# Performance work log

Hardware: AMD Instinct MI355X
Metric: run time of the kernel (lower is better)

The kernel has to match this reference:

```python
import jax, jax.numpy as jnp
import numpy as np

N_CODES, CODE_DIM = 1024, 256

def setup_inputs() -> dict:
    key = jax.random.key(0)
    k1, k2 = jax.random.split(key)
    z = jax.random.normal(k1, (32, 256, 32, 32), dtype=jnp.float32)
    # nn.init.uniform_(codebook.weight, -1/n_codes, 1/n_codes)
    codebook = jax.random.uniform(k2, (N_CODES, CODE_DIM), dtype=jnp.float32,
                                  minval=-1.0 / N_CODES, maxval=1.0 / N_CODES)
    return {"z": z, "codebook": codebook}

def reference(z, codebook):
    b, c, h, w = z.shape
    beta = 0.25
    z_flat = jnp.transpose(z, (0, 2, 3, 1)).reshape(-1, c)  # [B*H*W, C]
    z_sq = jnp.sum(z_flat * z_flat, axis=1, keepdims=True)   # [N,1]
    e_sq = jnp.sum(codebook * codebook, axis=1)              # [K]
    ze = z_flat @ codebook.T                                 # [N,K]
    dists = z_sq + e_sq[None, :] - 2.0 * ze
    indices = jnp.argmin(dists, axis=1)                      # [N]
    z_q = codebook[indices].reshape(b, h, w, c)
    z_q = jnp.transpose(z_q, (0, 3, 1, 2))                   # [B,C,H,W]
    z_q_st = z + jax.lax.stop_gradient(z_q - z)
    commitment = jnp.mean((jax.lax.stop_gradient(z) - z_q) ** 2)
    codebook_loss = jnp.mean((z - jax.lax.stop_gradient(z_q)) ** 2)
    vq_loss = codebook_loss + beta * commitment
    return z_q_st, vq_loss, indices.reshape(b, h, w)
```

## Files before the change

### kernel.cpp

```cpp
#include <hip/hip_runtime.h>
#include <math.h>

#define NROWS   32768
#define CDIM    256
#define KCODES  1024
#define ZQ_ELEMS 8388608

typedef short  bshort8 __attribute__((ext_vector_type(8)));
typedef float  f32x4   __attribute__((ext_vector_type(4)));

#define ESQ_OFF   0
#define ZSQH_OFF  1024
#define IDX_OFF   459776
#define LIST_OFF  492544
#define CNT_OFF   525312
#define ACC_OFF   525313
#define BHI_OFF   525328
#define BLO_OFF   656400


#define MARGIN_ABS 1.0e-4f

__device__ __forceinline__ ushort f2bf(float f) {
    union { float f; uint u; } v; v.f = f;
    uint lsb = (v.u >> 16) & 1u;
    return (ushort)((v.u + 0x7fffu + lsb) >> 16);
}
__device__ __forceinline__ float bf2f(ushort b) {
    union { uint u; float f; } v; v.u = ((uint)b) << 16;
    return v.f;
}

__global__ __launch_bounds__(256) void prep_kernel(const float* __restrict__ cb,
                                                   uint* __restrict__ Bhi, uint* __restrict__ Blo,
                                                   float* __restrict__ esq,
                                                   float* __restrict__ cbT) {
    const int blk = blockIdx.x, tid = threadIdx.x;
    if (blk < 128) {
        int F = blk * 256 + tid;
        int ct = F >> 9, ks = (F >> 6) & 7, ln = F & 63;
        int code = ct * 16 + (ln & 15);
        int k0 = ks * 32 + ((ln >> 4) << 3);
        const float* p = cb + (size_t)code * CDIM + k0;
        float4 va = *(const float4*)p;
        float4 vb = *(const float4*)(p + 4);
        float v[8] = {va.x, va.y, va.z, va.w, vb.x, vb.y, vb.z, vb.w};
        uint h[4], l[4];
#pragma unroll
        for (int d = 0; d < 4; ++d) {
            ushort h0 = f2bf(v[2*d]);   float r0 = v[2*d]   - bf2f(h0);
            ushort h1 = f2bf(v[2*d+1]); float r1 = v[2*d+1] - bf2f(h1);
            h[d] = (uint)h0 | ((uint)h1 << 16);
            l[d] = (uint)f2bf(r0) | ((uint)f2bf(r1) << 16);
        }
        *(uint4*)(Bhi + (size_t)F * 4) = make_uint4(h[0], h[1], h[2], h[3]);
        *(uint4*)(Blo + (size_t)F * 4) = make_uint4(l[0], l[1], l[2], l[3]);
    } else if (blk < 132) {
        int k = (blk - 128) * 256 + tid;
        const float* p = cb + (size_t)k * CDIM;
        float half_[2];
        for (int h = 0; h < 2; ++h) {
            const float* q = p + h * 128;
            float r8[8];
#pragma unroll
            for (int j = 0; j < 8; ++j) { float v = q[j]; r8[j] = __fmul_rn(v, v); }
            for (int i = 8; i < 128; i += 8) {
#pragma unroll
                for (int j = 0; j < 8; ++j) {
                    float v = q[i + j];
                    r8[j] = __fadd_rn(r8[j], __fmul_rn(v, v));
                }
            }
            half_[h] = __fadd_rn(__fadd_rn(__fadd_rn(r8[0], r8[1]), __fadd_rn(r8[2], r8[3])),
                                 __fadd_rn(__fadd_rn(r8[4], r8[5]), __fadd_rn(r8[6], r8[7])));
        }
        esq[k] = __fadd_rn(half_[0], half_[1]);
    } else {
        int base = (blk - 132) * 4096 + tid;
#pragma unroll
        for (int i = 0; i < 16; ++i) {
            int idx = base + i * 256;
            cbT[idx] = cb[(size_t)(idx & 1023) * CDIM + (idx >> 10)];
        }
    }
}

__global__ __launch_bounds__(512, 2) void main_mfma(const float* __restrict__ z,
                                                    const uint* __restrict__ Bhi,
                                                    const uint* __restrict__ Blo,
                                                    const float* __restrict__ esq,
                                                    float* __restrict__ zsqh,
                                                    float* __restrict__ oidxf,
                                                    int* __restrict__ idx_i,
                                                    int* __restrict__ list,
                                                    int* __restrict__ count) {
    __shared__ uint a_hi[8][4][64][4];
    __shared__ uint a_lo[8][4][64][4];
    __shared__ uint b_lds[8][2][4][64][4];
    __shared__ float esq_s[1024];
    __shared__ float zsq_s[64];
    __shared__ float m_b[8][64];
    __shared__ float m_s[8][64];
    __shared__ int   m_i[8][64];

    const int tid  = threadIdx.x;
    const int rg   = blockIdx.x;
    const int b    = rg >> 4;
    const int hw0  = (rg & 15) << 6;
    const int w    = tid >> 6;
    const int lane = tid & 63;

    {
        float2 e2 = *(const float2*)(esq + tid * 2);
        esq_s[tid * 2] = e2.x; esq_s[tid * 2 + 1] = e2.y;
    }

    {
        float* zt = (float*)&b_lds[0][0][0][0][0];
        float r8[8];
        const int zhalf = tid >> 6;
        const int zrow  = tid & 63;
        const int prt   = tid >> 6;
        const int plane = tid & 63;
        const int prow  = (plane & 15) + prt * 16;
        const int pkb   = (plane >> 4) << 3;

        for (int kc = 0; kc < 8; ++kc) {
            __syncthreads();
            {
                int cl = tid >> 4, h4 = tid & 15;
                float4 v = *(const float4*)(z + ((size_t)(b * 256 + kc * 32 + cl) << 10) + hw0 + h4 * 4);
                *(float4*)&zt[cl * 68 + h4 * 4] = v;
            }
            __syncthreads();
            if (tid < 128 && (kc >> 2) == zhalf) {
#pragma unroll
                for (int g = 0; g < 4; ++g)
#pragma unroll
                    for (int j = 0; j < 8; ++j) {
                        float v = zt[(g * 8 + j) * 68 + zrow];
                        float sq = __fmul_rn(v, v);
                        r8[j] = ((kc & 3) == 0 && g == 0) ? sq : __fadd_rn(r8[j], sq);
                    }
            }
            if (tid < 256) {
                uint hh[4], ll[4];
#pragma unroll
                for (int d = 0; d < 4; ++d) {
                    float v0 = zt[(pkb + 2*d)     * 68 + prow];
                    float v1 = zt[(pkb + 2*d + 1) * 68 + prow];
                    ushort x0 = f2bf(v0); float q0 = v0 - bf2f(x0);
                    ushort x1 = f2bf(v1); float q1 = v1 - bf2f(x1);
                    hh[d] = (uint)x0 | ((uint)x1 << 16);
                    ll[d] = (uint)f2bf(q0) | ((uint)f2bf(q1) << 16);
                }
                *(uint4*)&a_hi[kc][prt][plane][0] = make_uint4(hh[0], hh[1], hh[2], hh[3]);
                *(uint4*)&a_lo[kc][prt][plane][0] = make_uint4(ll[0], ll[1], ll[2], ll[3]);
            }
        }
        __syncthreads();
        if (tid < 128) {
            float hs = __fadd_rn(__fadd_rn(__fadd_rn(r8[0], r8[1]), __fadd_rn(r8[2], r8[3])),
                                 __fadd_rn(__fadd_rn(r8[4], r8[5]), __fadd_rn(r8[6], r8[7])));
            zt[zhalf * 64 + zrow] = hs;
            zsqh[zhalf * NROWS + rg * 64 + zrow] = hs;
        }
        __syncthreads();
        if (tid < 64) zsq_s[tid] = __fadd_rn(zt[tid], zt[64 + tid]);
        __syncthreads();
    }

#define GLDS(SRC, DST) __builtin_amdgcn_global_load_lds(                          \
        (const __attribute__((address_space(1))) void*)(SRC),                     \
        (__attribute__((address_space(3))) void*)(DST), 16, 0, 0)

    auto stage = [&](int t) {
        const int cg = t >> 3, ks = t & 7, buf = t & 1;
#pragma unroll
        for (int c = 0; c < 2; ++c) {
            int ct = w * 8 + cg * 2 + c;
            size_t F = ((size_t)(ct * 8 + ks) * 64 + lane);
            GLDS(Bhi + F * 4, &b_lds[w][buf][c * 2 + 0][0][0]);
            GLDS(Blo + F * 4, &b_lds[w][buf][c * 2 + 1][0][0]);
        }
    };

    float best[16], sec[16]; int bidx[16];
#pragma unroll
    for (int s = 0; s < 16; ++s) { best[s] = INFINITY; sec[s] = INFINITY; bidx[s] = 0; }

    f32x4 acc[4][2];

    asm volatile("s_waitcnt vmcnt(0)" ::: "memory");
    stage(0);

    for (int t = 0; t < 32; ++t) {
        const int ks = t & 7, cg = t >> 3, buf = t & 1;
        if (ks == 0) {
#pragma unroll
            for (int rt = 0; rt < 4; ++rt)
#pragma unroll
                for (int c = 0; c < 2; ++c) acc[rt][c] = (f32x4){0.f, 0.f, 0.f, 0.f};
        }
        if (t < 31) {
            stage(t + 1);
            asm volatile("s_waitcnt vmcnt(4)" ::: "memory");
        } else {
            asm volatile("s_waitcnt vmcnt(0)" ::: "memory");
        }
        __builtin_amdgcn_sched_barrier(0);

        {
            bshort8 bh[2], bl[2];
#pragma unroll
            for (int c = 0; c < 2; ++c) {
                bh[c] = *(const bshort8*)&b_lds[w][buf][c * 2 + 0][lane][0];
                bl[c] = *(const bshort8*)&b_lds[w][buf][c * 2 + 1][lane][0];
            }
#pragma unroll
            for (int rt = 0; rt < 4; ++rt) {
                bshort8 ah = *(const bshort8*)&a_hi[ks][rt][lane][0];
                bshort8 al = *(const bshort8*)&a_lo[ks][rt][lane][0];
#pragma unroll
                for (int c = 0; c < 2; ++c) {
                    acc[rt][c] = __builtin_amdgcn_mfma_f32_16x16x32_bf16(al, bh[c], acc[rt][c], 0, 0, 0);
                    acc[rt][c] = __builtin_amdgcn_mfma_f32_16x16x32_bf16(ah, bl[c], acc[rt][c], 0, 0, 0);
                    acc[rt][c] = __builtin_amdgcn_mfma_f32_16x16x32_bf16(ah, bh[c], acc[rt][c], 0, 0, 0);
                }
            }
        }

        if (ks == 7) {
            const int g = lane >> 4, cl = lane & 15;
#pragma unroll
            for (int c = 0; c < 2; ++c) {
                int ct = w * 8 + cg * 2 + c;
                int code = ct * 16 + cl;
                float es = esq_s[code];
#pragma unroll
                for (int rt = 0; rt < 4; ++rt)
#pragma unroll
                    for (int reg = 0; reg < 4; ++reg) {
                        int row_l = rt * 16 + g * 4 + reg;
                        float t1 = __fadd_rn(zsq_s[row_l], es);
                        float dd = __fadd_rn(t1, __fmul_rn(-2.0f, acc[rt][c][reg]));
                        int s = rt * 4 + reg;
                        if (dd < best[s]) { sec[s] = best[s]; best[s] = dd; bidx[s] = code; }
                        else if (dd < sec[s]) sec[s] = dd;
                    }
            }
        }
    }
#undef GLDS

#pragma unroll
    for (int mk = 1; mk <= 8; mk <<= 1) {
#pragma unroll
        for (int s = 0; s < 16; ++s) {
            float ob = __shfl_xor(best[s], mk, 64);
            float os = __shfl_xor(sec[s],  mk, 64);
            int   oi = __shfl_xor(bidx[s], mk, 64);
            float mx = fmaxf(best[s], ob);
            sec[s] = fminf(fminf(sec[s], os), mx);
            if (ob < best[s] || (ob == best[s] && oi < bidx[s])) { best[s] = ob; bidx[s] = oi; }
        }
    }
    if ((lane & 15) == 0) {
        const int g = lane >> 4;
#pragma unroll
        for (int s = 0; s < 16; ++s) {
            int rt = s >> 2, reg = s & 3;
            int row_l = rt * 16 + g * 4 + reg;
            m_b[w][row_l] = best[s]; m_s[w][row_l] = sec[s]; m_i[w][row_l] = bidx[s];
        }
    }
    __syncthreads();
    if (tid < 64) {
        float bb = INFINITY, ss = INFINITY; int bi = 0;
#pragma unroll
        for (int q = 0; q < 8; ++q) {
            float v = m_b[q][tid]; int vi = m_i[q][tid];
            if (v < bb || (v == bb && vi < bi)) { ss = bb; bb = v; bi = vi; }
            else ss = fminf(ss, v);
            ss = fminf(ss, m_s[q][tid]);
        }
        int row = rg * 64 + tid;
        if (ss <= bb + MARGIN_ABS) {
            int p = atomicAdd(count, 1);
            list[p] = row;
        } else {
            oidxf[row] = (float)bi;
            idx_i[row] = bi;
        }
    }
}

__global__ __launch_bounds__(256) void rescan_kernel(const float* __restrict__ z,
                                                     const float* __restrict__ cbT,
                                                     const float* __restrict__ esq,
                                                     const float* __restrict__ zsqh,
                                                     const int* __restrict__ list,
                                                     const int* __restrict__ count,
                                                     float* __restrict__ oidxf,
                                                     int* __restrict__ idx_i) {
    __shared__ float ct_lds[8][1024];
    __shared__ float z_lds[16][256];
    __shared__ float esq_lds[1024];
    const int tid = threadIdx.x, lane = tid & 63, w = tid >> 6;
    const int n = count[0];
#pragma unroll
    for (int i = 0; i < 4; ++i) esq_lds[i * 256 + tid] = esq[i * 256 + tid];

    for (int base = blockIdx.x * 16; base < n; base += gridDim.x * 16) {
        __syncthreads();
        for (int i = 0; i < 16; ++i) {
            int gi = base + i;
            int row = list[gi < n ? gi : n - 1];
            z_lds[i][tid] = z[((size_t)(row >> 10) * 256 + tid) * 1024 + (row & 1023)];
        }

        float acc[4][16];
#pragma unroll
        for (int r = 0; r < 4; ++r)
#pragma unroll
            for (int j = 0; j < 16; ++j) acc[r][j] = 0.0f;

        for (int kt = 0; kt < 32; ++kt) {
            __syncthreads();
#pragma unroll
            for (int u = 0; u < 8; ++u) {
                float4 v = *(const float4*)(cbT + (size_t)(kt * 8 + u) * 1024 + tid * 4);
                *(float4*)&ct_lds[u][tid * 4] = v;
            }
            __syncthreads();
#pragma unroll
            for (int k8 = 0; k8 < 8; ++k8) {
                float4 c[4];
#pragma unroll
                for (int j = 0; j < 4; ++j)
                    c[j] = *(const float4*)&ct_lds[k8][lane * 16 + j * 4];
#pragma unroll
                for (int r = 0; r < 4; ++r) {
                    float zv = z_lds[w * 4 + r][kt * 8 + k8];
                    acc[r][0]  = fmaf(zv, c[0].x, acc[r][0]);
                    acc[r][1]  = fmaf(zv, c[0].y, acc[r][1]);
                    acc[r][2]  = fmaf(zv, c[0].z, acc[r][2]);
                    acc[r][3]  = fmaf(zv, c[0].w, acc[r][3]);
                    acc[r][4]  = fmaf(zv, c[1].x, acc[r][4]);
                    acc[r][5]  = fmaf(zv, c[1].y, acc[r][5]);
                    acc[r][6]  = fmaf(zv, c[1].z, acc[r][6]);
                    acc[r][7]  = fmaf(zv, c[1].w, acc[r][7]);
                    acc[r][8]  = fmaf(zv, c[2].x, acc[r][8]);
                    acc[r][9]  = fmaf(zv, c[2].y, acc[r][9]);
                    acc[r][10] = fmaf(zv, c[2].z, acc[r][10]);
                    acc[r][11] = fmaf(zv, c[2].w, acc[r][11]);
                    acc[r][12] = fmaf(zv, c[3].x, acc[r][12]);
                    acc[r][13] = fmaf(zv, c[3].y, acc[r][13]);
                    acc[r][14] = fmaf(zv, c[3].z, acc[r][14]);
                    acc[r][15] = fmaf(zv, c[3].w, acc[r][15]);
                }
            }
        }

#pragma unroll
        for (int r = 0; r < 4; ++r) {
            int slot = w * 4 + r;
            int gi = base + slot;
            int row = list[gi < n ? gi : n - 1];
            float zs = __fadd_rn(zsqh[row], zsqh[NROWS + row]);
            float bv = INFINITY; int bi = 0;
#pragma unroll
            for (int j = 0; j < 16; ++j) {
                int code = lane * 16 + j;
                float dd = __fadd_rn(__fadd_rn(zs, esq_lds[code]), __fmul_rn(-2.0f, acc[r][j]));
                if (dd < bv) { bv = dd; bi = code; }
            }
#pragma unroll
            for (int mk = 1; mk <= 32; mk <<= 1) {
                float ob = __shfl_xor(bv, mk, 64);
                int   oi = __shfl_xor(bi, mk, 64);
                if (ob < bv || (ob == bv && oi < bi)) { bv = ob; bi = oi; }
            }
            if (lane == 0 && gi < n) { oidxf[row] = (float)bi; idx_i[row] = bi; }
        }
    }
}

__global__ __launch_bounds__(256) void gather_kernel(const float* __restrict__ z,
                                                     const float* __restrict__ cb,
                                                     const int* __restrict__ idx_i,
                                                     float* __restrict__ out0,
                                                     float* __restrict__ accum) {
    int tid   = threadIdx.x;
    int blk   = blockIdx.x;
    int b     = blk >> 5;
    int chunk = (blk >> 3) & 3;
    int cgrp  = blk & 7;
    int hw = chunk * 256 + tid;
    int n  = b * 1024 + hw;
    int code = idx_i[n];
    const float* cp = cb + (size_t)code * CDIM + cgrp * 32;
    float lsum = 0.0f;
    size_t base = (size_t)b * 262144 + hw + (size_t)(cgrp * 32) * 1024;
#pragma unroll
    for (int cc = 0; cc < 8; ++cc) {
        float4 q4 = *(const float4*)(cp + cc * 4);
        float qv[4] = {q4.x, q4.y, q4.z, q4.w};
#pragma unroll
        for (int u = 0; u < 4; ++u) {
            size_t off = base + (size_t)(cc * 4 + u) * 1024;
            float zv = z[off];
            out0[off] = qv[u];
            float dfr = zv - qv[u];
            lsum = fmaf(dfr, dfr, lsum);
        }
    }
#pragma unroll
    for (int mm = 32; mm >= 1; mm >>= 1) lsum += __shfl_down(lsum, mm, 64);
    __shared__ float red[4];
    int wv = tid >> 6, ln = tid & 63;
    if (ln == 0) red[wv] = lsum;
    __syncthreads();
    if (tid == 0) atomicAdd(accum, (red[0] + red[1]) + (red[2] + red[3]));
}

__global__ void finalize_loss(const float* __restrict__ accum, float* __restrict__ out_loss) {
    out_loss[0] = accum[0] * (1.25f / 8388608.0f);
}

extern "C" void kernel_launch(void* const* d_in, const int* in_sizes, int n_in,
                              void* d_out, int out_size, void* d_ws, size_t ws_size,
                              hipStream_t stream) {
    const float* z  = (const float*)d_in[0];
    const float* cb = (const float*)d_in[1];

    float* ws   = (float*)d_ws;
    float* esq  = ws + ESQ_OFF;
    float* zsqh = ws + ZSQH_OFF;
    int*   idx_i = (int*)(ws + IDX_OFF);
    int*   list = (int*)(ws + LIST_OFF);
    int*   cnt  = (int*)(ws + CNT_OFF);
    float* accum = ws + ACC_OFF;
    uint*  Bhi  = (uint*)(ws + BHI_OFF);
    uint*  Blo  = (uint*)(ws + BLO_OFF);

    float* out0     = (float*)d_out;
    float* out_loss = out0 + ZQ_ELEMS;
    float* out_idxf = out0 + ZQ_ELEMS + 1;

    float* cbT = out0;

    hipMemsetAsync(cnt, 0, 8, stream);

    prep_kernel <<<196, 256, 0, stream>>>(cb, Bhi, Blo, esq, cbT);
    main_mfma   <<<512, 512, 0, stream>>>(z, Bhi, Blo, esq, zsqh, out_idxf, idx_i, list, cnt);
    rescan_kernel<<<512, 256, 0, stream>>>(z, cbT, esq, zsqh, list, cnt, out_idxf, idx_i);
    gather_kernel<<<1024, 256, 0, stream>>>(z, cb, idx_i, out0, accum);
    finalize_loss<<<1, 1, 0, stream>>>(accum, out_loss);
}
```

Before: 227.6 us.

## Split block into row-halves and code-quarters, load codebook fragments directly to registers

The MFMA main loop is restructured. Each wave now covers 32 rows and 8 code tiles per pass, over two passes, instead of all 64 rows and 8 code tiles. Codebook hi/lo fragments are read straight from global memory into registers rather than staged through double-buffered LDS with global_load_lds and manual waitcnt. This shrinks LDS use (a dedicated small z-transpose buffer replaces the big B staging area) and halves the per-wave best/second registers, which may raise occupancy. In exchange, loads are no longer explicitly pipelined, and A-fragment reuse across code tiles changes, so global load latency may be exposed.

Measured after the change: 270.3 us. +18.8%, slower.

```diff
diff --git a/kernel.cpp b/kernel.cpp
--- a/kernel.cpp
+++ b/kernel.cpp
@@ -96,12 +96,12 @@
                                                     int* __restrict__ count) {
     __shared__ uint a_hi[8][4][64][4];
     __shared__ uint a_lo[8][4][64][4];
-    __shared__ uint b_lds[8][2][4][64][4];
+    __shared__ float zt[32 * 68];
     __shared__ float esq_s[1024];
     __shared__ float zsq_s[64];
-    __shared__ float m_b[8][64];
-    __shared__ float m_s[8][64];
-    __shared__ int   m_i[8][64];
+    __shared__ float m_b[4][64];
+    __shared__ float m_s[4][64];
+    __shared__ int   m_i[4][64];
 
     const int tid  = threadIdx.x;
     const int rg   = blockIdx.x;
@@ -109,6 +109,8 @@
     const int hw0  = (rg & 15) << 6;
     const int w    = tid >> 6;
     const int lane = tid & 63;
+    const int rh   = w >> 2;
+    const int cq   = w & 3;
 
     {
         float2 e2 = *(const float2*)(esq + tid * 2);
@@ -116,7 +118,6 @@
     }
 
     {
-        float* zt = (float*)&b_lds[0][0][0][0][0];
         float r8[8];
         const int zhalf = tid >> 6;
         const int zrow  = tid & 63;
@@ -170,93 +171,72 @@
         __syncthreads();
     }
 
-#define GLDS(SRC, DST) __builtin_amdgcn_global_load_lds(                          \
-        (const __attribute__((address_space(1))) void*)(SRC),                     \
-        (__attribute__((address_space(3))) void*)(DST), 16, 0, 0)
-
-    auto stage = [&](int t) {
-        const int cg = t >> 3, ks = t & 7, buf = t & 1;
-#pragma unroll
-        for (int c = 0; c < 2; ++c) {
-            int ct = w * 8 + cg * 2 + c;
-            size_t F = ((size_t)(ct * 8 + ks) * 64 + lane);
-            GLDS(Bhi + F * 4, &b_lds[w][buf][c * 2 + 0][0][0]);
-            GLDS(Blo + F * 4, &b_lds[w][buf][c * 2 + 1][0][0]);
-        }
-    };
-
-    float best[16], sec[16]; int bidx[16];
-#pragma unroll
-    for (int s = 0; s < 16; ++s) { best[s] = INFINITY; sec[s] = INFINITY; bidx[s] = 0; }
-
-    f32x4 acc[4][2];
-
-    asm volatile("s_waitcnt vmcnt(0)" ::: "memory");
-    stage(0);
-
-    for (int t = 0; t < 32; ++t) {
-        const int ks = t & 7, cg = t >> 3, buf = t & 1;
-        if (ks == 0) {
-#pragma unroll
-            for (int rt = 0; rt < 4; ++rt)
-#pragma unroll
-                for (int c = 0; c < 2; ++c) acc[rt][c] = (f32x4){0.f, 0.f, 0.f, 0.f};
-        }
-        if (t < 31) {
-            stage(t + 1);
-            asm volatile("s_waitcnt vmcnt(4)" ::: "memory");
-        } else {
-            asm volatile("s_waitcnt vmcnt(0)" ::: "memory");
-        }
-        __builtin_amdgcn_sched_barrier(0);
-
-        {
-            bshort8 bh[2], bl[2];
-#pragma unroll
-            for (int c = 0; c < 2; ++c) {
-                bh[c] = *(const bshort8*)&b_lds[w][buf][c * 2 + 0][lane][0];
-                bl[c] = *(const bshort8*)&b_lds[w][buf][c * 2 + 1][lane][0];
-            }
-#pragma unroll
-            for (int rt = 0; rt < 4; ++rt) {
-                bshort8 ah = *(const bshort8*)&a_hi[ks][rt][lane][0];
-                bshort8 al = *(const bshort8*)&a_lo[ks][rt][lane][0];
-#pragma unroll
-                for (int c = 0; c < 2; ++c) {
-                    acc[rt][c] = __builtin_amdgcn_mfma_f32_16x16x32_bf16(al, bh[c], acc[rt][c], 0, 0, 0);
-                    acc[rt][c] = __builtin_amdgcn_mfma_f32_16x16x32_bf16(ah, bl[c], acc[rt][c], 0, 0, 0);
-                    acc[rt][c] = __builtin_amdgcn_mfma_f32_16x16x32_bf16(ah, bh[c], acc[rt][c], 0, 0, 0);
+    float best[8], sec[8]; int bidx[8];
+#pragma unroll
+    for (int s = 0; s < 8; ++s) { best[s] = INFINITY; sec[s] = INFINITY; bidx[s] = 0; }
+
+    f32x4 acc[2][8];
+
+    for (int h = 0; h < 2; ++h) {
+        const int base_ct = h * 32 + cq * 8;
+#pragma unroll
+        for (int rt = 0; rt < 2; ++rt)
+#pragma unroll
+            for (int c = 0; c < 8; ++c) acc[rt][c] = (f32x4){0.f, 0.f, 0.f, 0.f};
+
+        for (int ks = 0; ks < 8; ++ks) {
+            bshort8 ah[2], al[2];
+#pragma unroll
+            for (int rt = 0; rt < 2; ++rt) {
+                ah[rt] = *(const bshort8*)&a_hi[ks][rh * 2 + rt][lane][0];
+                al[rt] = *(const bshort8*)&a_lo[ks][rh * 2 + rt][lane][0];
+            }
+#pragma unroll
+            for (int p = 0; p < 4; ++p) {
+                bshort8 bh[2], bl[2];
+#pragma unroll
+                for (int c2 = 0; c2 < 2; ++c2) {
+                    int ct = base_ct + p * 2 + c2;
+                    size_t F = ((size_t)(ct * 8 + ks) * 64 + lane) * 4;
+                    bh[c2] = *(const bshort8*)(Bhi + F);
+                    bl[c2] = *(const bshort8*)(Blo + F);
                 }
-            }
-        }
-
-        if (ks == 7) {
-            const int g = lane >> 4, cl = lane & 15;
-#pragma unroll
-            for (int c = 0; c < 2; ++c) {
-                int ct = w * 8 + cg * 2 + c;
-                int code = ct * 16 + cl;
-                float es = esq_s[code];
-#pragma unroll
-                for (int rt = 0; rt < 4; ++rt)
-#pragma unroll
-                    for (int reg = 0; reg < 4; ++reg) {
-                        int row_l = rt * 16 + g * 4 + reg;
-                        float t1 = __fadd_rn(zsq_s[row_l], es);
-                        float dd = __fadd_rn(t1, __fmul_rn(-2.0f, acc[rt][c][reg]));
-                        int s = rt * 4 + reg;
-                        if (dd < best[s]) { sec[s] = best[s]; best[s] = dd; bidx[s] = code; }
-                        else if (dd < sec[s]) sec[s] = dd;
+#pragma unroll
+                for (int rt = 0; rt < 2; ++rt)
+#pragma unroll
+                    for (int c2 = 0; c2 < 2; ++c2) {
+                        int c = p * 2 + c2;
+                        acc[rt][c] = __builtin_amdgcn_mfma_f32_16x16x32_bf16(al[rt], bh[c2], acc[rt][c], 0, 0, 0);
+                        acc[rt][c] = __builtin_amdgcn_mfma_f32_16x16x32_bf16(ah[rt], bl[c2], acc[rt][c], 0, 0, 0);
+                        acc[rt][c] = __builtin_amdgcn_mfma_f32_16x16x32_bf16(ah[rt], bh[c2], acc[rt][c], 0, 0, 0);
                     }
             }
         }
-    }
-#undef GLDS
+
+        const int g = lane >> 4, cl = lane & 15;
+#pragma unroll
+        for (int c = 0; c < 8; ++c) {
+            int ct = base_ct + c;
+            int code = ct * 16 + cl;
+            float es = esq_s[code];
+#pragma unroll
+            for (int rt = 0; rt < 2; ++rt)
+#pragma unroll
+                for (int reg = 0; reg < 4; ++reg) {
+                    int row_l = rh * 32 + rt * 16 + g * 4 + reg;
+                    float t1 = __fadd_rn(zsq_s[row_l], es);
+                    float dd = __fadd_rn(t1, __fmul_rn(-2.0f, acc[rt][c][reg]));
+                    int s = rt * 4 + reg;
+                    if (dd < best[s]) { sec[s] = best[s]; best[s] = dd; bidx[s] = code; }
+                    else if (dd < sec[s]) sec[s] = dd;
+                }
+        }
+    }
 
 #pragma unroll
     for (int mk = 1; mk <= 8; mk <<= 1) {
 #pragma unroll
-        for (int s = 0; s < 16; ++s) {
+        for (int s = 0; s < 8; ++s) {
             float ob = __shfl_xor(best[s], mk, 64);
             float os = __shfl_xor(sec[s],  mk, 64);
             int   oi = __shfl_xor(bidx[s], mk, 64);
@@ -268,17 +248,17 @@
     if ((lane & 15) == 0) {
         const int g = lane >> 4;
 #pragma unroll
-        for (int s = 0; s < 16; ++s) {
+        for (int s = 0; s < 8; ++s) {
             int rt = s >> 2, reg = s & 3;
-            int row_l = rt * 16 + g * 4 + reg;
-            m_b[w][row_l] = best[s]; m_s[w][row_l] = sec[s]; m_i[w][row_l] = bidx[s];
+            int row_l = rh * 32 + rt * 16 + g * 4 + reg;
+            m_b[cq][row_l] = best[s]; m_s[cq][row_l] = sec[s]; m_i[cq][row_l] = bidx[s];
         }
     }
     __syncthreads();
     if (tid < 64) {
         float bb = INFINITY, ss = INFINITY; int bi = 0;
 #pragma unroll
-        for (int q = 0; q < 8; ++q) {
+        for (int q = 0; q < 4; ++q) {
             float v = m_b[q][tid]; int vi = m_i[q][tid];
             if (v < bb || (v == bb && vi < bi)) { ss = bb; bb = v; bi = vi; }
             else ss = fminf(ss, v);
```
